# Optimization experiments

Hardware: AMD Instinct MI355X
Metric: run time of the kernel (lower is better)

The kernel has to match this reference:

```python
import jax, jax.numpy as jnp
import numpy as np

B, L, D, K, C = 4, 1024, 1024, 20, 21  # images, proposals/img, feat dim, dict size, classes


def setup_inputs() -> dict:
    key = jax.random.key(0)
    ks = jax.random.split(key, 6)
    return {
        "x": jax.random.normal(ks[0], (B, L, D), jnp.float32),
        "dic": jax.random.normal(ks[1], (K, D), jnp.float32),
        "prior": jax.random.uniform(ks[2], (K,), jnp.float32),
        "Wy_w": jax.random.normal(ks[3], (C, D), jnp.float32) * 0.02,
        "Wy_b": jnp.zeros((C,), jnp.float32),
        "Wz_w": jax.random.normal(ks[4], (C, D), jnp.float32) * 0.02,
        "Wz_b": jnp.zeros((C,), jnp.float32),
        "cs_w": jax.random.normal(ks[5], (C, 2 * D), jnp.float32) * 0.01,
        "cs_b": jnp.zeros((C,), jnp.float32),
    }


def reference(x, dic, prior, Wy_w, Wy_b, Wz_w, Wz_b, cs_w, cs_b):
    # attention over a small class dictionary, then pairwise outer-sum causal logits.
    scale = 1.0 / jnp.sqrt(jnp.asarray(C, x.dtype))  # embedding_size ** 0.5 == sqrt(21)
    zd = dic @ Wz_w.T + Wz_b  # [K, C] Wz(dic), shared across images

    def per_image(y):  # y: [L, D]
        att = jax.nn.softmax(((y @ Wy_w.T + Wy_b) @ zd.T) * scale, axis=1)  # [L, K]
        # prior @ (att[:, :, None] * dic[None]) == (att * prior) @ dic
        z = (att * prior[None, :]) @ dic  # [L, D]
        # causal_score(cat(y_i, z_j)) == y_i @ W[:, :D].T + z_j @ W[:, D:].T + b
        ly = y @ cs_w[:, :D].T            # [L, C]
        lz = z @ cs_w[:, D:].T + cs_b     # [L, C]
        return (ly[:, None, :] + lz[None, :, :]).reshape(L * L, C)  # [L*L, C]

    return jax.vmap(per_image)(x)  # [B, L*L, C]
```

## Files before the change

kernel.cpp:

```cpp
#include <hip/hip_runtime.h>
#include <math.h>

#define BB 4
#define LL 1024
#define DD 1024
#define KK 20
#define CC 21
#define LC (LL * CC)
#define NQ (LC / 4)

typedef float vf4    __attribute__((ext_vector_type(4)));
typedef short bf16x8 __attribute__((ext_vector_type(8)));
typedef float f32x4  __attribute__((ext_vector_type(4)));

__device__ __forceinline__ unsigned short f2bf(float f) {
    unsigned int u = __builtin_bit_cast(unsigned int, f);
    u += 0x7FFFu + ((u >> 16) & 1u);
    return (unsigned short)(u >> 16);
}

__device__ __forceinline__ bf16x8 cvt8(float4 a, float4 b) {
    bf16x8 r;
    r[0] = (short)f2bf(a.x); r[1] = (short)f2bf(a.y);
    r[2] = (short)f2bf(a.z); r[3] = (short)f2bf(a.w);
    r[4] = (short)f2bf(b.x); r[5] = (short)f2bf(b.y);
    r[6] = (short)f2bf(b.z); r[7] = (short)f2bf(b.w);
    return r;
}

__device__ __forceinline__ void gload_lds16(const float* g, float* l) {
    __builtin_amdgcn_global_load_lds(
        (const __attribute__((address_space(1))) unsigned int*)g,
        (__attribute__((address_space(3))) unsigned int*)l, 16, 0, 0);
}

__device__ __forceinline__ float wave_reduce_sum(float v) {
    #pragma unroll
    for (int off = 1; off < 64; off <<= 1)
        v += __shfl_xor(v, off, 64);
    return v;
}

#define DOT4(a, b) ((a).x*(b).x + (a).y*(b).y + (a).z*(b).z + (a).w*(b).w)

__global__ __launch_bounds__(64) void k0_zdM(
    const float* __restrict__ dic,
    const float* __restrict__ Wz_w, const float* __restrict__ Wz_b,
    const float* __restrict__ cs_w,
    float* __restrict__ zd, float* __restrict__ M)
{
    int blk = blockIdx.x;
    int lane = threadIdx.x;
    bool isM = (blk >= KK * CC);
    int e2 = isM ? blk - KK * CC : blk;
    int k = e2 / CC, c = e2 % CC;
    const float4* a4 = reinterpret_cast<const float4*>(dic + (size_t)k * DD);
    const float*  w  = isM ? (cs_w + (size_t)c * (2 * DD) + DD) : (Wz_w + (size_t)c * DD);
    const float4* w4 = reinterpret_cast<const float4*>(w);
    float p = 0.f;
    #pragma unroll
    for (int i = 0; i < 4; ++i) {
        float4 av = a4[lane + 64 * i];
        float4 wv = w4[lane + 64 * i];
        p += DOT4(av, wv);
    }
    p = wave_reduce_sum(p);
    if (lane == 0) {
        if (isM) M[e2] = p;
        else     zd[e2] = p + Wz_b[c];
    }
}

__global__ __launch_bounds__(512) void k1_mfma(
    const float* __restrict__ x,
    const float* __restrict__ prior,
    const float* __restrict__ Wy_w, const float* __restrict__ Wy_b,
    const float* __restrict__ cs_w, const float* __restrict__ cs_b,
    const float* __restrict__ zd, const float* __restrict__ M,
    float* __restrict__ ly_ws, float* __restrict__ lz_ws)
{
    const int tid  = threadIdx.x;
    const int wid  = tid >> 6;
    const int lane = tid & 63;
    const int fr   = lane & 15;
    const int kg   = lane >> 4;
    const int r0   = blockIdx.x * 16;

    __shared__ float zds[KK * CC];
    __shared__ float Ms[KK * CC];
    __shared__ float pr[KK];
    __shared__ float bias[2 * CC];
    __shared__ float xT[16 * 1024];
    __shared__ float pacc[8 * 16 * 49];

    {
        const float* gbase = x + (size_t)r0 * DD;
        #pragma unroll
        for (int i = 0; i < 8; ++i) {
            int chunk = wid * 8 + i;
            gload_lds16(gbase + chunk * 256 + lane * 4, &xT[chunk * 256]);
        }
    }

    for (int i = tid; i < KK * CC; i += 512) { zds[i] = zd[i]; Ms[i] = M[i]; }
    if (tid < KK) pr[tid] = prior[tid];
    if (tid < CC) { bias[tid] = Wy_b[tid]; bias[CC + tid] = cs_b[tid]; }
    __syncthreads();

    const float* w0p = Wy_w + (size_t)fr * DD;
    const float* w1p = (fr < 5) ? (Wy_w + (size_t)(fr + 16) * DD)
                                : (cs_w + (size_t)(fr - 5) * (2 * DD));
    const bool  z2  = (fr >= 10);
    const float* w2p = z2 ? cs_w
                          : (cs_w + (size_t)(fr + 11) * (2 * DD));

    const int kbase = wid * 128;
    const int koff  = kbase + kg * 8;
    const float* ap = &xT[fr * 1024 + koff];

    f32x4 acc0 = {0.f, 0.f, 0.f, 0.f};
    f32x4 acc1 = {0.f, 0.f, 0.f, 0.f};
    f32x4 acc2 = {0.f, 0.f, 0.f, 0.f};

    #pragma unroll
    for (int ks = 0; ks < 4; ++ks) {
        int o = koff + ks * 32;
        float4 a0 = *reinterpret_cast<const float4*>(ap + ks * 32);
        float4 a1 = *reinterpret_cast<const float4*>(ap + ks * 32 + 4);
        float4 b0a = *reinterpret_cast<const float4*>(w0p + o);
        float4 b0b = *reinterpret_cast<const float4*>(w0p + o + 4);
        float4 b1a = *reinterpret_cast<const float4*>(w1p + o);
        float4 b1b = *reinterpret_cast<const float4*>(w1p + o + 4);
        float4 b2a = *reinterpret_cast<const float4*>(w2p + o);
        float4 b2b = *reinterpret_cast<const float4*>(w2p + o + 4);
        if (z2) { b2a = make_float4(0.f,0.f,0.f,0.f); b2b = make_float4(0.f,0.f,0.f,0.f); }
        bf16x8 af = cvt8(a0, a1);
        bf16x8 b0 = cvt8(b0a, b0b);
        bf16x8 b1 = cvt8(b1a, b1b);
        bf16x8 b2 = cvt8(b2a, b2b);
        acc0 = __builtin_amdgcn_mfma_f32_16x16x32_bf16(af, b0, acc0, 0, 0, 0);
        acc1 = __builtin_amdgcn_mfma_f32_16x16x32_bf16(af, b1, acc1, 0, 0, 0);
        acc2 = __builtin_amdgcn_mfma_f32_16x16x32_bf16(af, b2, acc2, 0, 0, 0);
    }

    #pragma unroll
    for (int j = 0; j < 4; ++j) {
        float* pw = pacc + ((wid * 16) + kg * 4 + j) * 49;
        pw[fr]      = acc0[j];
        pw[16 + fr] = acc1[j];
        pw[32 + fr] = acc2[j];
    }
    __syncthreads();

    #pragma unroll
    for (int p = 0; p < 2; ++p) {
        int o = tid + p * 512;
        if (o < 768) {
            int row = o / 48, col = o % 48;
            float s = 0.f;
            #pragma unroll
            for (int w = 0; w < 8; ++w) s += pacc[((w * 16) + row) * 49 + col];
            pacc[row * 49 + col] = s;
        }
    }
    __syncthreads();

    if (tid < 64) {
        const float* f = pacc + fr * 49;
        const float scale = 0.21821789023599238f;
        float s[KK];
        float m = -1e30f;
        #pragma unroll
        for (int k = 0; k < KK; ++k) {
            float t = 0.f;
            #pragma unroll
            for (int c = 0; c < CC; ++c) t += (f[c] + bias[c]) * zds[k * CC + c];
            s[k] = t * scale;
            m = fmaxf(m, s[k]);
        }
        float sum = 0.f;
        #pragma unroll
        for (int k = 0; k < KK; ++k) { s[k] = expf(s[k] - m); sum += s[k]; }
        float inv = 1.f / sum;
        float wk[KK];
        #pragma unroll
        for (int k = 0; k < KK; ++k) wk[k] = s[k] * inv * pr[k];

        size_t rr = (size_t)(r0 + fr);
        for (int c = kg; c < CC; c += 4) {
            float lzv = bias[CC + c];
            #pragma unroll
            for (int k = 0; k < KK; ++k) lzv += wk[k] * Ms[k * CC + c];
            ly_ws[rr * CC + c] = f[CC + c];
            lz_ws[rr * CC + c] = lzv;
        }
    }
}

__global__ __launch_bounds__(512) void k2_outer(
    const float* __restrict__ ly_ws, const float* __restrict__ lz_ws,
    float* __restrict__ out)
{
    int tid = threadIdx.x;
    int blk = blockIdx.x;
    int b  = blk >> 8;
    int i0 = (blk & 255) << 2;

    __shared__ vf4 lyp4[4 * CC];
    {
        float* lyp = reinterpret_cast<float*>(lyp4);
        if (tid < 4 * 84) {
            int i = tid / 84, f = tid % 84;
            lyp[i * 84 + f] = ly_ws[(size_t)(b * LL + i0 + i) * CC + (f % 21)];
        }
    }
    const float* lzp = lz_ws + (size_t)b * LC;
    vf4 lzv[11];
    #pragma unroll
    for (int it = 0; it < 11; ++it) {
        int idx = tid + it * 512;
        lzv[it] = (idx < NQ) ? *reinterpret_cast<const vf4*>(lzp + (size_t)idx * 4)
                             : (vf4){0.f, 0.f, 0.f, 0.f};
    }
    __syncthreads();
    int g0 = tid % 21;

    #pragma unroll
    for (int i = 0; i < 4; ++i) {
        float* op = out + (size_t)(b * LL + i0 + i) * LC;
        const vf4* lyp_i = lyp4 + i * CC;
        int g = g0;
        #pragma unroll
        for (int it = 0; it < 11; ++it) {
            int idx = tid + it * 512;
            if (idx < NQ) {
                *reinterpret_cast<vf4*>(op + (size_t)idx * 4) = lzv[it] + lyp_i[g];
            }
            g += 8; if (g >= 21) g -= 21;
        }
    }
}

extern "C" void kernel_launch(void* const* d_in, const int* in_sizes, int n_in,
                              void* d_out, int out_size, void* d_ws, size_t ws_size,
                              hipStream_t stream)
{
    const float* x     = (const float*)d_in[0];
    const float* dic   = (const float*)d_in[1];
    const float* prior = (const float*)d_in[2];
    const float* Wy_w  = (const float*)d_in[3];
    const float* Wy_b  = (const float*)d_in[4];
    const float* Wz_w  = (const float*)d_in[5];
    const float* Wz_b  = (const float*)d_in[6];
    const float* cs_w  = (const float*)d_in[7];
    const float* cs_b  = (const float*)d_in[8];
    float* out = (float*)d_out;

    float* ws = (float*)d_ws;
    float* zd = ws;
    float* M  = ws + 512;
    float* ly = ws + 1024;
    float* lz = ly + BB * LL * CC;

    k0_zdM <<<dim3(2 * KK * CC),  dim3(64),  0, stream>>>(dic, Wz_w, Wz_b, cs_w, zd, M);
    k1_mfma<<<dim3(BB * LL / 16), dim3(512), 0, stream>>>(x, prior, Wy_w, Wy_b, cs_w, cs_b,
                                                          zd, M, ly, lz);
    k2_outer<<<dim3(BB * LL / 4), dim3(512), 0, stream>>>(ly, lz, out);
}
```

Measured before the change: 90.49 us.

## Fuse zd/M precompute into main MFMA kernel, computing per block redundantly

Removes the separate k0 kernel that computed zd = dic·Wz^T and M = dic·cs_w[:,D:]^T. Each of the 256 blocks of the main kernel now loads dic into LDS as bf16 and computes both small matrices with MFMA before the main projection. This saves one kernel launch and the dependency between launches. In exchange, every block redundantly reads dic and Wz and does extra MFMA and reduction passes, adds about 41KB of LDS (which may lower occupancy), and computes zd/M in bf16 instead of fp32.

```diff
diff --git a/kernel.cpp b/kernel.cpp
--- a/kernel.cpp
+++ b/kernel.cpp
@@ -8,6 +8,7 @@
 #define CC 21
 #define LC (LL * CC)
 #define NQ (LC / 4)
+#define DS 1032
 
 typedef float vf4    __attribute__((ext_vector_type(4)));
 typedef short bf16x8 __attribute__((ext_vector_type(8)));
@@ -34,49 +35,13 @@
         (__attribute__((address_space(3))) unsigned int*)l, 16, 0, 0);
 }
 
-__device__ __forceinline__ float wave_reduce_sum(float v) {
-    #pragma unroll
-    for (int off = 1; off < 64; off <<= 1)
-        v += __shfl_xor(v, off, 64);
-    return v;
-}
-
-#define DOT4(a, b) ((a).x*(b).x + (a).y*(b).y + (a).z*(b).z + (a).w*(b).w)
-
-__global__ __launch_bounds__(64) void k0_zdM(
+__global__ __launch_bounds__(512) void k1_fused(
+    const float* __restrict__ x,
     const float* __restrict__ dic,
-    const float* __restrict__ Wz_w, const float* __restrict__ Wz_b,
-    const float* __restrict__ cs_w,
-    float* __restrict__ zd, float* __restrict__ M)
-{
-    int blk = blockIdx.x;
-    int lane = threadIdx.x;
-    bool isM = (blk >= KK * CC);
-    int e2 = isM ? blk - KK * CC : blk;
-    int k = e2 / CC, c = e2 % CC;
-    const float4* a4 = reinterpret_cast<const float4*>(dic + (size_t)k * DD);
-    const float*  w  = isM ? (cs_w + (size_t)c * (2 * DD) + DD) : (Wz_w + (size_t)c * DD);
-    const float4* w4 = reinterpret_cast<const float4*>(w);
-    float p = 0.f;
-    #pragma unroll
-    for (int i = 0; i < 4; ++i) {
-        float4 av = a4[lane + 64 * i];
-        float4 wv = w4[lane + 64 * i];
-        p += DOT4(av, wv);
-    }
-    p = wave_reduce_sum(p);
-    if (lane == 0) {
-        if (isM) M[e2] = p;
-        else     zd[e2] = p + Wz_b[c];
-    }
-}
-
-__global__ __launch_bounds__(512) void k1_mfma(
-    const float* __restrict__ x,
     const float* __restrict__ prior,
     const float* __restrict__ Wy_w, const float* __restrict__ Wy_b,
+    const float* __restrict__ Wz_w, const float* __restrict__ Wz_b,
     const float* __restrict__ cs_w, const float* __restrict__ cs_b,
-    const float* __restrict__ zd, const float* __restrict__ M,
     float* __restrict__ ly_ws, float* __restrict__ lz_ws)
 {
     const int tid  = threadIdx.x;
@@ -91,6 +56,7 @@
     __shared__ float pr[KK];
     __shared__ float bias[2 * CC];
     __shared__ float xT[16 * 1024];
+    __shared__ unsigned short dicT[20 * DS];
     __shared__ float pacc[8 * 16 * 49];
 
     {
@@ -102,68 +68,132 @@
         }
     }
 
-    for (int i = tid; i < KK * CC; i += 512) { zds[i] = zd[i]; Ms[i] = M[i]; }
+    #pragma unroll
+    for (int i = 0; i < 10; ++i) {
+        int f = tid + i * 512;
+        int row  = f >> 8;
+        int col4 = f & 255;
+        float4 v = *reinterpret_cast<const float4*>(dic + (size_t)row * DD + col4 * 4);
+        unsigned int lo = (unsigned int)f2bf(v.x) | ((unsigned int)f2bf(v.y) << 16);
+        unsigned int hi = (unsigned int)f2bf(v.z) | ((unsigned int)f2bf(v.w) << 16);
+        *reinterpret_cast<uint2*>(&dicT[row * DS + col4 * 4]) = make_uint2(lo, hi);
+    }
+
     if (tid < KK) pr[tid] = prior[tid];
     if (tid < CC) { bias[tid] = Wy_b[tid]; bias[CC + tid] = cs_b[tid]; }
     __syncthreads();
 
-    const float* w0p = Wy_w + (size_t)fr * DD;
-    const float* w1p = (fr < 5) ? (Wy_w + (size_t)(fr + 16) * DD)
-                                : (cs_w + (size_t)(fr - 5) * (2 * DD));
-    const bool  z2  = (fr >= 10);
-    const float* w2p = z2 ? cs_w
-                          : (cs_w + (size_t)(fr + 11) * (2 * DD));
-
     const int kbase = wid * 128;
     const int koff  = kbase + kg * 8;
-    const float* ap = &xT[fr * 1024 + koff];
-
-    f32x4 acc0 = {0.f, 0.f, 0.f, 0.f};
-    f32x4 acc1 = {0.f, 0.f, 0.f, 0.f};
-    f32x4 acc2 = {0.f, 0.f, 0.f, 0.f};
-
-    #pragma unroll
-    for (int ks = 0; ks < 4; ++ks) {
-        int o = koff + ks * 32;
-        float4 a0 = *reinterpret_cast<const float4*>(ap + ks * 32);
-        float4 a1 = *reinterpret_cast<const float4*>(ap + ks * 32 + 4);
-        float4 b0a = *reinterpret_cast<const float4*>(w0p + o);
-        float4 b0b = *reinterpret_cast<const float4*>(w0p + o + 4);
-        float4 b1a = *reinterpret_cast<const float4*>(w1p + o);
-        float4 b1b = *reinterpret_cast<const float4*>(w1p + o + 4);
-        float4 b2a = *reinterpret_cast<const float4*>(w2p + o);
-        float4 b2b = *reinterpret_cast<const float4*>(w2p + o + 4);
-        if (z2) { b2a = make_float4(0.f,0.f,0.f,0.f); b2b = make_float4(0.f,0.f,0.f,0.f); }
-        bf16x8 af = cvt8(a0, a1);
-        bf16x8 b0 = cvt8(b0a, b0b);
-        bf16x8 b1 = cvt8(b1a, b1b);
-        bf16x8 b2 = cvt8(b2a, b2b);
-        acc0 = __builtin_amdgcn_mfma_f32_16x16x32_bf16(af, b0, acc0, 0, 0, 0);
-        acc1 = __builtin_amdgcn_mfma_f32_16x16x32_bf16(af, b1, acc1, 0, 0, 0);
-        acc2 = __builtin_amdgcn_mfma_f32_16x16x32_bf16(af, b2, acc2, 0, 0, 0);
-    }
-
-    #pragma unroll
-    for (int j = 0; j < 4; ++j) {
-        float* pw = pacc + ((wid * 16) + kg * 4 + j) * 49;
-        pw[fr]      = acc0[j];
-        pw[16 + fr] = acc1[j];
-        pw[32 + fr] = acc2[j];
-    }
-    __syncthreads();
-
-    #pragma unroll
-    for (int p = 0; p < 2; ++p) {
-        int o = tid + p * 512;
-        if (o < 768) {
-            int row = o / 48, col = o % 48;
-            float s = 0.f;
-            #pragma unroll
-            for (int w = 0; w < 8; ++w) s += pacc[((w * 16) + row) * 49 + col];
-            pacc[row * 49 + col] = s;
-        }
-    }
-    __syncthreads();
+
+    {
+        const float* v0p = Wz_w + (size_t)fr * DD;
+        const float* v1p = (fr < 5) ? (Wz_w + (size_t)(fr + 16) * DD)
+                                    : (cs_w + (size_t)(fr - 5) * (2 * DD) + DD);
+        const bool  vz2 = (fr >= 10);
+        const float* v2p = vz2 ? cs_w
+                               : (cs_w + (size_t)(fr + 11) * (2 * DD) + DD);
+
+        #pragma unroll
+        for (int t = 0; t < 2; ++t) {
+            int arow = (t == 0) ? fr : ((16 + fr > 19) ? 19 : 16 + fr);
+            const unsigned short* ap2 = dicT + (size_t)arow * DS + koff;
+
+            f32x4 e0 = {0.f,0.f,0.f,0.f};
+            f32x4 e1 = {0.f,0.f,0.f,0.f};
+            f32x4 e2 = {0.f,0.f,0.f,0.f};
+            #pragma unroll
+            for (int ks = 0; ks < 4; ++ks) {
+                int o = koff + ks * 32;
+                bf16x8 af = *reinterpret_cast<const bf16x8*>(ap2 + ks * 32);
+                float4 b0a = *reinterpret_cast<const float4*>(v0p + o);
+                float4 b0b = *reinterpret_cast<const float4*>(v0p + o + 4);
+                float4 b1a = *reinterpret_cast<const float4*>(v1p + o);
+                float4 b1b = *reinterpret_cast<const float4*>(v1p + o + 4);
+                float4 b2a = *reinterpret_cast<const float4*>(v2p + o);
+                float4 b2b = *reinterpret_cast<const float4*>(v2p + o + 4);
+                if (vz2) { b2a = make_float4(0,0,0,0); b2b = make_float4(0,0,0,0); }
+                e0 = __builtin_amdgcn_mfma_f32_16x16x32_bf16(af, cvt8(b0a,b0b), e0, 0,0,0);
+                e1 = __builtin_amdgcn_mfma_f32_16x16x32_bf16(af, cvt8(b1a,b1b), e1, 0,0,0);
+                e2 = __builtin_amdgcn_mfma_f32_16x16x32_bf16(af, cvt8(b2a,b2b), e2, 0,0,0);
+            }
+            #pragma unroll
+            for (int j = 0; j < 4; ++j) {
+                float* pw = pacc + ((wid * 16) + kg * 4 + j) * 49;
+                pw[fr]      = e0[j];
+                pw[16 + fr] = e1[j];
+                pw[32 + fr] = e2[j];
+            }
+            __syncthreads();
+
+            int nout = (t == 0) ? 16 * 42 : 4 * 42;
+            for (int o = tid; o < nout; o += 512) {
+                int row = o / 42, col = o % 42;
+                float s = 0.f;
+                #pragma unroll
+                for (int w = 0; w < 8; ++w) s += pacc[((w * 16) + row) * 49 + col];
+                int k = t * 16 + row;
+                if (col < CC) zds[k * CC + col] = s + Wz_b[col];
+                else          Ms[k * CC + (col - CC)] = s;
+            }
+            __syncthreads();
+        }
+    }
+
+    {
+        const float* w0p = Wy_w + (size_t)fr * DD;
+        const float* w1p = (fr < 5) ? (Wy_w + (size_t)(fr + 16) * DD)
+                                    : (cs_w + (size_t)(fr - 5) * (2 * DD));
+        const bool  z2  = (fr >= 10);
+        const float* w2p = z2 ? cs_w
+                              : (cs_w + (size_t)(fr + 11) * (2 * DD));
+
+        const float* ap = &xT[fr * 1024 + koff];
+
+        f32x4 acc0 = {0.f,0.f,0.f,0.f};
+        f32x4 acc1 = {0.f,0.f,0.f,0.f};
+        f32x4 acc2 = {0.f,0.f,0.f,0.f};
+
+        #pragma unroll
+        for (int ks = 0; ks < 4; ++ks) {
+            int o = koff + ks * 32;
+            float4 a0 = *reinterpret_cast<const float4*>(ap + ks * 32);
+            float4 a1 = *reinterpret_cast<const float4*>(ap + ks * 32 + 4);
+            float4 b0a = *reinterpret_cast<const float4*>(w0p + o);
+            float4 b0b = *reinterpret_cast<const float4*>(w0p + o + 4);
+            float4 b1a = *reinterpret_cast<const float4*>(w1p + o);
+            float4 b1b = *reinterpret_cast<const float4*>(w1p + o + 4);
+            float4 b2a = *reinterpret_cast<const float4*>(w2p + o);
+            float4 b2b = *reinterpret_cast<const float4*>(w2p + o + 4);
+            if (z2) { b2a = make_float4(0,0,0,0); b2b = make_float4(0,0,0,0); }
+            bf16x8 af = cvt8(a0, a1);
+            acc0 = __builtin_amdgcn_mfma_f32_16x16x32_bf16(af, cvt8(b0a,b0b), acc0, 0,0,0);
+            acc1 = __builtin_amdgcn_mfma_f32_16x16x32_bf16(af, cvt8(b1a,b1b), acc1, 0,0,0);
+            acc2 = __builtin_amdgcn_mfma_f32_16x16x32_bf16(af, cvt8(b2a,b2b), acc2, 0,0,0);
+        }
+
+        #pragma unroll
+        for (int j = 0; j < 4; ++j) {
+            float* pw = pacc + ((wid * 16) + kg * 4 + j) * 49;
+            pw[fr]      = acc0[j];
+            pw[16 + fr] = acc1[j];
+            pw[32 + fr] = acc2[j];
+        }
+        __syncthreads();
+
+        #pragma unroll
+        for (int p = 0; p < 2; ++p) {
+            int o = tid + p * 512;
+            if (o < 768) {
+                int row = o / 48, col = o % 48;
+                float s = 0.f;
+                #pragma unroll
+                for (int w = 0; w < 8; ++w) s += pacc[((w * 16) + row) * 49 + col];
+                pacc[row * 49 + col] = s;
+            }
+        }
+        __syncthreads();
+    }
 
     if (tid < 64) {
         const float* f = pacc + fr * 49;
@@ -257,13 +287,11 @@
     float* out = (float*)d_out;
 
     float* ws = (float*)d_ws;
-    float* zd = ws;
-    float* M  = ws + 512;
-    float* ly = ws + 1024;
+    float* ly = ws;
     float* lz = ly + BB * LL * CC;
 
-    k0_zdM <<<dim3(2 * KK * CC),  dim3(64),  0, stream>>>(dic, Wz_w, Wz_b, cs_w, zd, M);
-    k1_mfma<<<dim3(BB * LL / 16), dim3(512), 0, stream>>>(x, prior, Wy_w, Wy_b, cs_w, cs_b,
-                                                          zd, M, ly, lz);
-    k2_outer<<<dim3(BB * LL / 4), dim3(512), 0, stream>>>(ly, lz, out);
-}
+    k1_fused<<<dim3(BB * LL / 16), dim3(512), 0, stream>>>(x, dic, prior,
+                                                           Wy_w, Wy_b, Wz_w, Wz_b,
+                                                           cs_w, cs_b, ly, lz);
+    k2_outer<<<dim3(BB * LL / 4),  dim3(512), 0, stream>>>(ly, lz, out);
+}
```

New measurement: 93.05 us. 1.03x slower.
